# Kernel tuning notes

Measured on AMD Instinct MI355X. Metric: run time of the kernel, lower is better.

## Reference

```python
import jax, jax.numpy as jnp
import numpy as np

N, E, Nd, D, F = 100000, 400000, 4096, 512, 8000
EMB = 300
NUM_LAYERS = 5


def setup_inputs() -> dict:
    key = jax.random.key(0)
    ks = iter(jax.random.split(key, 24))
    x = jax.random.randint(next(ks), (N, 2), 0, 3)
    edge_index = jax.random.randint(next(ks), (2, E), 0, N)
    edge_attr = jax.random.randint(next(ks), (E, 2), 0, 3)
    dangling_idx = jax.random.randint(next(ks), (Nd,), 0, N)
    frag_batch = jnp.sort(jax.random.randint(next(ks), (N,), 0, F))
    dangling_edge_index = jax.random.randint(next(ks), (2, D), 0, Nd)
    drop_edge_attr = jax.random.randint(next(ks), (D, 2), 0, 3)
    p = lambda shape: jax.random.normal(next(ks), shape, jnp.float32) * 0.02
    return dict(
        x=x, edge_index=edge_index, edge_attr=edge_attr,
        dangling_idx=dangling_idx, frag_batch=frag_batch,
        dangling_edge_index=dangling_edge_index, drop_edge_attr=drop_edge_attr,
        atom_emb1=p((120, EMB)), atom_emb2=p((3, EMB)),
        gin_ee1=p((NUM_LAYERS, 6, EMB)), gin_ee2=p((NUM_LAYERS, 3, EMB)),
        W1=p((NUM_LAYERS, EMB, 2 * EMB)), b1=jnp.zeros((NUM_LAYERS, 2 * EMB), jnp.float32),
        W2=p((NUM_LAYERS, 2 * EMB, EMB)), b2=jnp.zeros((NUM_LAYERS, EMB), jnp.float32),
        bn_g=jnp.ones((NUM_LAYERS, EMB), jnp.float32), bn_b=jnp.zeros((NUM_LAYERS, EMB), jnp.float32),
        E1=p((6, 4 * EMB * EMB)), E2=p((3, 4 * EMB * EMB)),
    )


def _gnn(x, edge_index, edge_attr, atom_emb1, atom_emb2,
         gin_ee1, gin_ee2, W1, b1, W2, b2, bn_g, bn_b):
    # node features from two categorical embeddings
    h = atom_emb1[x[:, 0]] + atom_emb2[x[:, 1]]  # [N, EMB]
    src, dst = edge_index[0], edge_index[1]
    for l in range(NUM_LAYERS):
        ee = gin_ee1[l][edge_attr[:, 0]] + gin_ee2[l][edge_attr[:, 1]]  # [E, EMB]
        aggr = jax.ops.segment_sum(h[src] + ee, dst, num_segments=N)
        # self-loops with edge_attr = (4, 0)
        aggr = aggr + h + gin_ee1[l][4] + gin_ee2[l][0]
        h = jax.nn.relu(aggr @ W1[l] + b1[l]) @ W2[l] + b2[l]  # GIN MLP
        # BatchNorm1d (training-mode batch statistics), eps=1e-5
        mean = h.mean(axis=0)
        var = h.var(axis=0)
        h = (h - mean) * jax.lax.rsqrt(var + 1e-5) * bn_g[l] + bn_b[l]
        if l < NUM_LAYERS - 1:
            h = jax.nn.relu(h)
    return h


def reference(x, edge_index, edge_attr, dangling_idx, frag_batch,
              dangling_edge_index, drop_edge_attr,
              atom_emb1, atom_emb2, gin_ee1, gin_ee2,
              W1, b1, W2, b2, bn_g, bn_b, E1, E2):
    h = _gnn(x, edge_index, edge_attr, atom_emb1, atom_emb2,
             gin_ee1, gin_ee2, W1, b1, W2, b2, bn_g, bn_b)  # [N, EMB]
    dangling_out = h[dangling_idx]  # [Nd, EMB]
    # global_mean_pool over fragments
    seg_sum = jax.ops.segment_sum(h, frag_batch, num_segments=F)
    cnt = jax.ops.segment_sum(jnp.ones((N, 1), h.dtype), frag_batch, num_segments=F)
    frag_mean = seg_sum / jnp.maximum(cnt, 1.0)
    frag_out = frag_mean[frag_batch][dangling_idx]  # [Nd, EMB]
    out = jnp.concatenate([dangling_out, frag_out], axis=1) / EMB  # [Nd, 2*EMB]
    out0 = out[dangling_edge_index[0]]  # [D, 2*EMB]
    # per-edge dynamic weight matrices [D, 2*EMB, 2*EMB]
    pm = (E1[drop_edge_attr[:, 0]] + E2[drop_edge_attr[:, 1]]).reshape(D, 2 * EMB, 2 * EMB)
    out0 = jnp.einsum('dk,dkm->dm', out0, pm)
    out1 = out[dangling_edge_index[1]]
    out2 = jnp.roll(out1, 1, axis=0)  # shift_k fixed to 1 for determinism
    logits = jnp.concatenate([jnp.sum(out0 * out1, axis=1),
                              jnp.sum(out0 * out2, axis=1)], axis=0)  # [2*D]
    return logits
```

## Files before the change

kernel.cpp:

```cpp
#include <hip/hip_runtime.h>
#include <hip/hip_bf16.h>
#include <stdint.h>

#define NN 100000
#define EE 400000
#define ND 4096
#define DD 512
#define FF 8000
#define EMB 300
#define HID 600
#define NL 5
#define TCH 50176
#define MPAD 100096

typedef unsigned short u16;
typedef _Float16 f16x8 __attribute__((ext_vector_type(8)));
typedef float f32x4 __attribute__((ext_vector_type(4)));

static __device__ inline u16 f2h(float v) {
    union { _Float16 h; u16 u; } c; c.h = (_Float16)v; return c.u;
}
static __device__ inline float h2f(u16 u) {
    union { u16 u; _Float16 h; } c; c.u = u; return (float)c.h;
}
static __device__ inline uint32_t pk2(float a, float b) {
    return (uint32_t)f2h(a) | ((uint32_t)f2h(b) << 16);
}
static __device__ inline int loff(int row, int cb) {
    return row * 32 + ((cb ^ ((row >> 1) & 3)) * 8);
}

static __global__ void k_init_h(const int* __restrict__ x, const float* __restrict__ ae1,
                                const float* __restrict__ ae2, uint32_t* __restrict__ h) {
    int idx = blockIdx.x * 256 + threadIdx.x;
    if (idx >= NN * 160) return;
    int n = idx / 160, cw = idx - n * 160;
    int c = 2 * cw;
    int x0 = x[2 * n], x1 = x[2 * n + 1];
    float v0 = 0.f, v1 = 0.f;
    if (c < EMB)     v0 = ae1[x0 * EMB + c] + ae2[x1 * EMB + c];
    if (c + 1 < EMB) v1 = ae1[x0 * EMB + c + 1] + ae2[x1 * EMB + c + 1];
    h[idx] = pk2(v0, v1);
}

static __global__ void k_count(const int* __restrict__ ei, const int* __restrict__ ea,
                               int* __restrict__ deg, int* __restrict__ cnt1, int* __restrict__ cnt2) {
    int e = blockIdx.x * 256 + threadIdx.x;
    if (e >= EE) return;
    int dst = ei[EE + e];
    atomicAdd(&deg[dst], 1);
    atomicAdd(&cnt1[dst * 3 + ea[2 * e]], 1);
    atomicAdd(&cnt2[dst * 3 + ea[2 * e + 1]], 1);
}

static __global__ void k_scan1(const int* __restrict__ in, int* __restrict__ incl,
                               int* __restrict__ bsum, int L) {
    __shared__ int s[256];
    int t = threadIdx.x, i = blockIdx.x * 256 + t;
    int v = (i < L) ? in[i] : 0;
    s[t] = v; __syncthreads();
    for (int o = 1; o < 256; o <<= 1) {
        int xv = (t >= o) ? s[t - o] : 0; __syncthreads();
        s[t] += xv; __syncthreads();
    }
    if (i < L) incl[i] = s[t];
    if (t == 255) bsum[blockIdx.x] = s[255];
}

static __global__ void k_scan2(const int* __restrict__ bsum, int* __restrict__ boff, int nb) {
    __shared__ int s[1024];
    int t = threadIdx.x;
    int v = (t < nb) ? bsum[t] : 0;
    s[t] = v; __syncthreads();
    for (int o = 1; o < 1024; o <<= 1) {
        int xv = (t >= o) ? s[t - o] : 0; __syncthreads();
        s[t] += xv; __syncthreads();
    }
    if (t < nb) boff[t] = s[t] - v;
}

static __global__ void k_scan3(const int* __restrict__ in, const int* __restrict__ incl,
                               const int* __restrict__ boff, int* __restrict__ op,
                               int* __restrict__ cursor, int L) {
    int i = blockIdx.x * 256 + threadIdx.x;
    if (i >= L) return;
    int ex = incl[i] - in[i] + boff[i / 256];
    op[i] = ex;
    if (cursor) cursor[i] = ex;
    if (i == L - 1) op[L] = ex + in[i];
}

static __global__ void k_scatter(const int* __restrict__ ei, int* __restrict__ cursor,
                                 int* __restrict__ col) {
    int e = blockIdx.x * 256 + threadIdx.x;
    if (e >= EE) return;
    int dst = ei[EE + e], src = ei[e];
    int p = atomicAdd(&cursor[dst], 1);
    col[p] = src;
}

static __global__ void k_aggr(const u16* __restrict__ h, u16* __restrict__ ag,
                              const int* __restrict__ rowptr, const int* __restrict__ col,
                              const int* __restrict__ cnt1, const int* __restrict__ cnt2,
                              const float* __restrict__ ge1l, const float* __restrict__ ge2l,
                              const float* __restrict__ scv, int relu) {
    __shared__ float se[7 * 320];
    for (int idx = threadIdx.x; idx < 7 * 320; idx += 256) {
        int g = idx / 320, c = idx - g * 320;
        float v = 0.f;
        if (c < EMB) {
            if (g < 3) v = ge1l[g * EMB + c];
            else if (g < 6) v = ge2l[(g - 3) * EMB + c];
            else v = ge1l[4 * EMB + c] + ge2l[c];
        }
        se[idx] = v;
    }
    __syncthreads();
    int wv = threadIdx.x >> 6, lane = threadIdx.x & 63;
    int n = blockIdx.x * 4 + wv;
    if (n >= NN) return;
    float c1a = (float)cnt1[n * 3], c1b = (float)cnt1[n * 3 + 1], c1c = (float)cnt1[n * 3 + 2];
    float c2a = (float)cnt2[n * 3], c2b = (float)cnt2[n * 3 + 1], c2c = (float)cnt2[n * 3 + 2];

    int cw[3];
    float sc0[3], sh0[3], sc1[3], sh1[3];
    float acc0[3], acc1[3];
    const uint32_t* hn = (const uint32_t*)(h + (size_t)n * 320);
#pragma unroll
    for (int j = 0; j < 3; j++) {
        cw[j] = lane + 64 * j;
        if (cw[j] < 160) {
            int c = 2 * cw[j];
            if (scv) { sc0[j] = scv[c]; sh0[j] = scv[320 + c]; sc1[j] = scv[c + 1]; sh1[j] = scv[321 + c]; }
            else     { sc0[j] = 1.f; sh0[j] = 0.f; sc1[j] = 1.f; sh1[j] = 0.f; }
            uint32_t hv = hn[cw[j]];
            float v0 = h2f((u16)(hv & 0xffff)) * sc0[j] + sh0[j];
            float v1 = h2f((u16)(hv >> 16))    * sc1[j] + sh1[j];
            if (relu) { v0 = fmaxf(v0, 0.f); v1 = fmaxf(v1, 0.f); }
            acc0[j] = v0 + se[6 * 320 + c]
                    + c1a * se[c] + c1b * se[320 + c] + c1c * se[640 + c]
                    + c2a * se[960 + c] + c2b * se[1280 + c] + c2c * se[1600 + c];
            acc1[j] = v1 + se[6 * 320 + c + 1]
                    + c1a * se[c + 1] + c1b * se[321 + c] + c1c * se[641 + c]
                    + c2a * se[961 + c] + c2b * se[1281 + c] + c2c * se[1601 + c];
        }
    }
    int beg = rowptr[n], end = rowptr[n + 1];
    for (int p = beg; p < end; ++p) {
        const uint32_t* hr = (const uint32_t*)(h + (size_t)col[p] * 320);
#pragma unroll
        for (int j = 0; j < 3; j++) {
            if (cw[j] < 160) {
                uint32_t hv = hr[cw[j]];
                float v0 = h2f((u16)(hv & 0xffff)) * sc0[j] + sh0[j];
                float v1 = h2f((u16)(hv >> 16))    * sc1[j] + sh1[j];
                if (relu) { v0 = fmaxf(v0, 0.f); v1 = fmaxf(v1, 0.f); }
                acc0[j] += v0; acc1[j] += v1;
            }
        }
    }
    uint32_t* ao = (uint32_t*)(ag + (size_t)n * 320);
#pragma unroll
    for (int j = 0; j < 3; j++)
        if (cw[j] < 160) ao[cw[j]] = pk2(acc0[j], acc1[j]);
}

static __global__ void k_packW1(const float* __restrict__ W1, u16* __restrict__ W1p) {
    int idx = blockIdx.x * 256 + threadIdx.x;
    const int per = 640 * 320;
    if (idx >= NL * per) return;
    int l = idx / per, rem = idx % per;
    int n = rem / 320, k = rem % 320;
    float v = (k < EMB && n < HID) ? W1[(size_t)l * EMB * HID + (size_t)k * HID + n] : 0.f;
    W1p[idx] = f2h(v);
}

static __global__ void k_packW2(const float* __restrict__ W2, u16* __restrict__ W2p) {
    int idx = blockIdx.x * 256 + threadIdx.x;
    const int per = 384 * 640;
    if (idx >= NL * per) return;
    int l = idx / per, rem = idx % per;
    int n = rem / 640, k = rem % 640;
    float v = (k < HID && n < EMB) ? W2[(size_t)l * HID * EMB + (size_t)k * EMB + n] : 0.f;
    W2p[idx] = f2h(v);
}

static __global__ void k_packb(const float* __restrict__ b1, const float* __restrict__ b2,
                               float* __restrict__ b1p, float* __restrict__ b2p) {
    int idx = blockIdx.x * 256 + threadIdx.x;
    if (idx < NL * 640) {
        int l = idx / 640, n = idx % 640;
        b1p[idx] = (n < HID) ? b1[l * HID + n] : 0.f;
    } else if (idx < NL * 640 + NL * 384) {
        int j = idx - NL * 640;
        int l = j / 384, n = j % 384;
        b2p[j] = (n < EMB) ? b2[l * EMB + n] : 0.f;
    }
}

static __global__ void k_precompMt(const float* __restrict__ E1, const float* __restrict__ E2,
                                   u16* __restrict__ Mpt) {
    __shared__ float sT[32][33];
    int p = blockIdx.x, mt = blockIdx.y, kt = blockIdx.z;
    int a = p / 3, b = p % 3;
    const float* e1 = E1 + (size_t)a * 360000;
    const float* e2 = E2 + (size_t)b * 360000;
    int tx = threadIdx.x & 31, ty = threadIdx.x >> 5;
#pragma unroll
    for (int it = 0; it < 4; it++) {
        int k = kt * 32 + ty + it * 8;
        int m = mt * 32 + tx;
        float v = 0.f;
        if (k < HID && m < HID) v = e1[k * HID + m] + e2[k * HID + m];
        sT[ty + it * 8][tx] = v;
    }
    __syncthreads();
#pragma unroll
    for (int it = 0; it < 4; it++) {
        int m = mt * 32 + ty + it * 8;
        int k = kt * 32 + tx;
        Mpt[(size_t)p * 640 * 640 + (size_t)m * 640 + k] = f2h(sT[tx][ty + it * 8]);
    }
}

template <int MODE>
static __global__ __launch_bounds__(256) void k_mfma(
        const u16* __restrict__ A, const u16* __restrict__ B,
        const float* __restrict__ bias, u16* __restrict__ Out, int Mc,
        float* __restrict__ colsum, float* __restrict__ colsq) {
    constexpr int BM    = (MODE == 1) ? 128 : 64;
    constexpr int STR   = (MODE == 1) ? 320 : 640;
    constexpr int STRO  = (MODE == 1) ? 640 : 320;
    constexpr int NSTEP = (MODE == 1) ? 10 : 20;
    constexpr int MF = 4;
    constexpr int NF = (MODE == 1) ? 4 : 2;

    __shared__ __align__(16) u16 sA[BM * 32];
    __shared__ __align__(16) u16 sB[128 * 32];

    int tid = threadIdx.x;
    int lane = tid & 63, wv = tid >> 6;
    int wm = (MODE == 1) ? (wv >> 1) : 0;
    int wn = (MODE == 1) ? (wv & 1) : wv;
    int m0 = blockIdx.y * BM;
    int n0 = blockIdx.x * 128;
    int sr = tid >> 2, scb = tid & 3;

    uint4 rA0, rA1, rB0, rB1;
    auto do_load = [&](int ks) {
        int kk = ks * 32;
        const u16* as = A + (size_t)(m0 + sr) * STR + kk + scb * 8;
        rA0 = *(const uint4*)as;
        if (MODE == 1) rA1 = *(const uint4*)(as + (size_t)64 * STR);
        const u16* bs = B + (size_t)(n0 + sr) * STR + kk + scb * 8;
        rB0 = *(const uint4*)bs;
        rB1 = *(const uint4*)(bs + (size_t)64 * STR);
    };
    do_load(0);

    f32x4 acc[MF][NF];
#pragma unroll
    for (int i = 0; i < MF; i++)
#pragma unroll
        for (int j = 0; j < NF; j++) {
            acc[i][j][0] = 0.f; acc[i][j][1] = 0.f; acc[i][j][2] = 0.f; acc[i][j][3] = 0.f;
        }

    int lrow = lane & 15, lcb = lane >> 4;
    for (int ks = 0; ks < NSTEP; ++ks) {
        __syncthreads();
        *(uint4*)&sA[loff(sr, scb)] = rA0;
        if (MODE == 1) *(uint4*)&sA[loff(sr + 64, scb)] = rA1;
        *(uint4*)&sB[loff(sr, scb)] = rB0;
        *(uint4*)&sB[loff(sr + 64, scb)] = rB1;
        __syncthreads();
        if (ks + 1 < NSTEP) do_load(ks + 1);
        f16x8 af[MF], bfr[NF];
#pragma unroll
        for (int mf = 0; mf < MF; ++mf) {
            int r = wm * 64 + mf * 16 + lrow;
            af[mf] = *(const f16x8*)&sA[loff(r, lcb)];
        }
#pragma unroll
        for (int nf = 0; nf < NF; ++nf) {
            int r = wn * (NF * 16) + nf * 16 + lrow;
            bfr[nf] = *(const f16x8*)&sB[loff(r, lcb)];
        }
#pragma unroll
        for (int mf = 0; mf < MF; ++mf)
#pragma unroll
            for (int nf = 0; nf < NF; ++nf)
                acc[mf][nf] = __builtin_amdgcn_mfma_f32_16x16x32_f16(af[mf], bfr[nf], acc[mf][nf], 0, 0, 0);
    }

    int lrow4 = (lane >> 4) * 4, lcol = lane & 15;
    if (MODE == 1) {
#pragma unroll
        for (int mf = 0; mf < MF; ++mf)
#pragma unroll
            for (int nf = 0; nf < NF; ++nf) {
                int colg = n0 + wn * 64 + nf * 16 + lcol;
                float bv = bias[colg];
#pragma unroll
                for (int rg = 0; rg < 4; ++rg) {
                    int rowl = m0 + wm * 64 + mf * 16 + lrow4 + rg;
                    float v = fmaxf(acc[mf][nf][rg] + bv, 0.f);
                    Out[(size_t)rowl * STRO + colg] = f2h(v);
                }
            }
    } else {
#pragma unroll
        for (int nf = 0; nf < NF; ++nf) {
            int colg = n0 + wn * 32 + nf * 16 + lcol;
            float bv = bias[colg];
            float s = 0.f, q = 0.f;
#pragma unroll
            for (int mf = 0; mf < MF; ++mf)
#pragma unroll
                for (int rg = 0; rg < 4; ++rg) {
                    int rowl = m0 + mf * 16 + lrow4 + rg;
                    float v = acc[mf][nf][rg] + bv;
                    if (rowl < Mc) {
                        s += v; q += v * v;
                        if (colg < EMB) Out[(size_t)rowl * STRO + colg] = f2h(v);
                    }
                }
            s += __shfl_xor(s, 16); s += __shfl_xor(s, 32);
            q += __shfl_xor(q, 16); q += __shfl_xor(q, 32);
            if (lane < 16) { atomicAdd(&colsum[colg], s); atomicAdd(&colsq[colg], q); }
        }
    }
}

static __global__ void k_bnfinal(const float* __restrict__ colsum, const float* __restrict__ colsq,
                                 const float* __restrict__ g, const float* __restrict__ b,
                                 float* __restrict__ scv) {
    int c = threadIdx.x;
    if (c >= 320) return;
    if (c >= EMB) { scv[c] = 0.f; scv[320 + c] = 0.f; return; }
    float mean = colsum[c] * (1.f / NN);
    float var = colsq[c] * (1.f / NN) - mean * mean;
    float rs = rsqrtf(var + 1e-5f);
    float sc = rs * g[c];
    scv[c] = sc;
    scv[320 + c] = b[c] - mean * sc;
}

static __global__ void k_fragcnt(const int* __restrict__ fb, int* __restrict__ fcnt) {
    int i = blockIdx.x * 256 + threadIdx.x;
    if (i >= NN) return;
    atomicAdd(&fcnt[fb[i]], 1);
}

static __global__ void k_fragmean(const u16* __restrict__ h, const int* __restrict__ fstart,
                                  const float* __restrict__ scv, float* __restrict__ fm) {
    int wv = threadIdx.x >> 6, lane = threadIdx.x & 63;
    int f = blockIdx.x * 4 + wv;
    if (f >= FF) return;
    int beg = fstart[f], end = fstart[f + 1];
    float inv = (end > beg) ? 1.f / (float)(end - beg) : 0.f;
    float a0[3], a1[3]; int cw[3];
#pragma unroll
    for (int j = 0; j < 3; j++) { cw[j] = lane + 64 * j; a0[j] = 0.f; a1[j] = 0.f; }
    for (int r = beg; r < end; ++r) {
        const uint32_t* hr = (const uint32_t*)(h + (size_t)r * 320);
#pragma unroll
        for (int j = 0; j < 3; j++)
            if (cw[j] < 160) {
                uint32_t hv = hr[cw[j]];
                a0[j] += h2f((u16)(hv & 0xffff)); a1[j] += h2f((u16)(hv >> 16));
            }
    }
#pragma unroll
    for (int j = 0; j < 3; j++) {
        int c = 2 * cw[j];
        if (c < EMB)
            fm[(size_t)f * EMB + c] = (end > beg) ? (a0[j] * inv * scv[c] + scv[320 + c]) : 0.f;
        if (c + 1 < EMB)
            fm[(size_t)f * EMB + c + 1] = (end > beg) ? (a1[j] * inv * scv[c + 1] + scv[321 + c]) : 0.f;
    }
}

static __global__ void k_build_out(const u16* __restrict__ h, const float* __restrict__ fm,
                                   const int* __restrict__ didx, const int* __restrict__ fb,
                                   const float* __restrict__ scv, u16* __restrict__ outb16) {
    int idx = blockIdx.x * 256 + threadIdx.x;
    if (idx >= ND * 640) return;
    int d = idx / 640, c = idx - d * 640;
    int n = didx[d];
    float v = 0.f;
    if (c < EMB)          v = (h2f(h[(size_t)n * 320 + c]) * scv[c] + scv[320 + c]) * (1.f / EMB);
    else if (c < 2 * EMB) v = fm[(size_t)fb[n] * EMB + (c - EMB)] * (1.f / EMB);
    outb16[idx] = f2h(v);
}

static __global__ void k_bucket(const int* __restrict__ dea, int* __restrict__ eord,
                                int* __restrict__ tm, int* __restrict__ ntl) {
    __shared__ int cnt[9], off[9], cur[9];
    __shared__ short pe[DD];
    int tid = threadIdx.x;
    for (int i = tid; i < 768; i += 256) eord[i] = -1;
    if (tid < 9) { cnt[tid] = 0; cur[tid] = 0; }
    __syncthreads();
    for (int e = tid; e < DD; e += 256) {
        int p = dea[2 * e] * 3 + dea[2 * e + 1];
        pe[e] = (short)p;
        atomicAdd(&cnt[p], 1);
    }
    __syncthreads();
    if (tid == 0) {
        int o = 0, tt = 0;
        for (int p = 0; p < 9; p++) {
            off[p] = o;
            int nt = (cnt[p] + 15) >> 4;
            for (int t = 0; t < nt; t++) { tm[2 * tt] = p; tm[2 * tt + 1] = o + 16 * t; tt++; }
            o += nt * 16;
        }
        *ntl = tt;
    }
    __syncthreads();
    for (int e = tid; e < DD; e += 256) {
        int p = pe[e];
        int slot = off[p] + atomicAdd(&cur[p], 1);
        eord[slot] = e;
    }
}

static __global__ void k_vgather(const u16* __restrict__ outb16, const int* __restrict__ eord,
                                 const int* __restrict__ dei, u16* __restrict__ Vg) {
    int idx = blockIdx.x * 256 + threadIdx.x;
    if (idx >= 768 * 80) return;
    int slot = idx / 80, cb = idx - slot * 80;
    int d = eord[slot];
    uint4 v = {0u, 0u, 0u, 0u};
    if (d >= 0) v = *(const uint4*)&outb16[(size_t)dei[d] * 640 + cb * 8];
    *(uint4*)&Vg[(size_t)slot * 640 + cb * 8] = v;
}

static __global__ __launch_bounds__(256) void k_out0m(
        const u16* __restrict__ Vg, const u16* __restrict__ Mpt,
        const int* __restrict__ tm, const int* __restrict__ ntl,
        const int* __restrict__ eord, float* __restrict__ o0) {
    int bx = blockIdx.x;
    if (bx >= *ntl) return;
    int p = tm[2 * bx], row0 = tm[2 * bx + 1];
    __shared__ __align__(16) u16 sA[16 * 32];
    __shared__ __align__(16) u16 sB[640 * 32];
    int tid = threadIdx.x, lane = tid & 63, wv = tid >> 6;
    const u16* Bb = Mpt + (size_t)p * 640 * 640;
    f32x4 acc[10];
#pragma unroll
    for (int j = 0; j < 10; j++) { acc[j][0]=0.f; acc[j][1]=0.f; acc[j][2]=0.f; acc[j][3]=0.f; }
    int lrow = lane & 15, lcb = lane >> 4;
    for (int ks = 0; ks < 20; ks++) {
        int kk = ks * 32;
        __syncthreads();
        if (tid < 64) {
            int row = tid >> 2, cb = tid & 3;
            *(uint4*)&sA[loff(row, cb)] = *(const uint4*)&Vg[(size_t)(row0 + row) * 640 + kk + cb * 8];
        }
#pragma unroll
        for (int j = 0; j < 10; j++) {
            int i = tid + j * 256, row = i >> 2, cb = i & 3;
            *(uint4*)&sB[loff(row, cb)] = *(const uint4*)&Bb[(size_t)row * 640 + kk + cb * 8];
        }
        __syncthreads();
        f16x8 af = *(const f16x8*)&sA[loff(lrow, lcb)];
#pragma unroll
        for (int nf = 0; nf < 10; nf++) {
            f16x8 bf = *(const f16x8*)&sB[loff(wv * 160 + nf * 16 + lrow, lcb)];
            acc[nf] = __builtin_amdgcn_mfma_f32_16x16x32_f16(af, bf, acc[nf], 0, 0, 0);
        }
    }
    int lrow4 = (lane >> 4) * 4, lcol = lane & 15;
#pragma unroll
    for (int nf = 0; nf < 10; nf++) {
        int col = wv * 160 + nf * 16 + lcol;
#pragma unroll
        for (int rg = 0; rg < 4; rg++) {
            int row = lrow4 + rg;
            int e = eord[row0 + row];
            if (e >= 0 && col < HID) o0[(size_t)e * 640 + col] = acc[nf][rg];
        }
    }
}

static __global__ void k_logits(const float* __restrict__ o0, const u16* __restrict__ outb16,
                                const int* __restrict__ dei, float* __restrict__ dout) {
    int d = blockIdx.x;
    int tid = threadIdx.x, lane = tid & 63;
    int which = tid >> 6;
    int dsel = which ? (d + DD - 1) % DD : d;
    const float* a = o0 + (size_t)d * 640;
    const u16* bv = outb16 + (size_t)dei[DD + dsel] * 640;
    float s = 0.f;
    for (int c = lane; c < HID; c += 64) s += a[c] * h2f(bv[c]);
    for (int o = 32; o > 0; o >>= 1) s += __shfl_down(s, o);
    if (lane == 0) dout[which ? DD + d : d] = s;
}

extern "C" void kernel_launch(void* const* d_in, const int* in_sizes, int n_in,
                              void* d_out, int out_size, void* d_ws, size_t ws_size,
                              hipStream_t stream) {
    const int* x    = (const int*)d_in[0];
    const int* ei   = (const int*)d_in[1];
    const int* ea   = (const int*)d_in[2];
    const int* didx = (const int*)d_in[3];
    const int* fb   = (const int*)d_in[4];
    const int* dei  = (const int*)d_in[5];
    const int* dea  = (const int*)d_in[6];
    const float* ae1 = (const float*)d_in[7];
    const float* ae2 = (const float*)d_in[8];
    const float* ge1 = (const float*)d_in[9];
    const float* ge2 = (const float*)d_in[10];
    const float* W1  = (const float*)d_in[11];
    const float* b1  = (const float*)d_in[12];
    const float* W2  = (const float*)d_in[13];
    const float* b2  = (const float*)d_in[14];
    const float* bng = (const float*)d_in[15];
    const float* bnb = (const float*)d_in[16];
    const float* E1  = (const float*)d_in[17];
    const float* E2  = (const float*)d_in[18];
    float* dout = (float*)d_out;

    char* w = (char*)d_ws;
    auto alloc = [&](size_t bytes) -> void* {
        void* p = (void*)w;
        w += (bytes + 255) & ~(size_t)255;
        return p;
    };
    u16* h   = (u16*)alloc((size_t)MPAD * 320 * 2);
    u16* ag  = (u16*)alloc((size_t)MPAD * 320 * 2);
    u16* t   = (u16*)alloc((size_t)TCH * 640 * 2);
    u16* W1p = (u16*)alloc((size_t)NL * 640 * 320 * 2);
    u16* W2p = (u16*)alloc((size_t)NL * 384 * 640 * 2);
    u16* Mpt = (u16*)alloc((size_t)9 * 640 * 640 * 2);
    float* b1p = (float*)alloc((size_t)NL * 640 * 4);
    float* b2p = (float*)alloc((size_t)NL * 384 * 4);
    int* rowptr = (int*)alloc((size_t)(NN + 1) * 4);
    int* cursor = (int*)alloc((size_t)NN * 4);
    int* col    = (int*)alloc((size_t)EE * 4);
    int* deg    = (int*)alloc((size_t)NN * 4);
    int* cnt1   = (int*)alloc((size_t)NN * 3 * 4);
    int* cnt2   = (int*)alloc((size_t)NN * 3 * 4);
    int* incl   = (int*)alloc((size_t)NN * 4);
    int* bsum   = (int*)alloc(4096);
    int* boff   = (int*)alloc(4096);
    int* fcnt   = (int*)alloc((size_t)FF * 4);
    int* fstart = (int*)alloc((size_t)(FF + 1) * 4);
    float* colsum = (float*)alloc(384 * 4);
    float* colsq  = (float*)alloc(384 * 4);
    float* scv    = (float*)alloc(640 * 4);
    int* eord = (int*)alloc(768 * 4);
    int* tm   = (int*)alloc(96 * 4);
    int* ntl  = (int*)alloc(256);
    char* ov = (char*)t;
    auto oalloc = [&](size_t bytes) -> void* {
        void* p = (void*)ov;
        ov += (bytes + 255) & ~(size_t)255;
        return p;
    };
    float* fragmean = (float*)oalloc((size_t)FF * EMB * 4);
    u16* outb16     = (u16*)oalloc((size_t)ND * 640 * 2);
    float* o0       = (float*)oalloc((size_t)DD * 640 * 4);
    u16* Vg         = (u16*)oalloc((size_t)768 * 640 * 2);

    hipMemsetAsync(deg, 0, (size_t)NN * 4, stream);
    hipMemsetAsync(cnt1, 0, (size_t)NN * 3 * 4, stream);
    hipMemsetAsync(cnt2, 0, (size_t)NN * 3 * 4, stream);
    hipMemsetAsync(fcnt, 0, (size_t)FF * 4, stream);

    k_packW1<<<(NL * 640 * 320 + 255) / 256, 256, 0, stream>>>(W1, W1p);
    k_packW2<<<(NL * 384 * 640 + 255) / 256, 256, 0, stream>>>(W2, W2p);
    k_packb<<<(NL * (640 + 384) + 255) / 256, 256, 0, stream>>>(b1, b2, b1p, b2p);
    k_precompMt<<<dim3(9, 20, 20), 256, 0, stream>>>(E1, E2, Mpt);
    k_bucket<<<1, 256, 0, stream>>>(dea, eord, tm, ntl);

    k_init_h<<<(NN * 160 + 255) / 256, 256, 0, stream>>>(x, ae1, ae2, (uint32_t*)h);
    k_count<<<(EE + 255) / 256, 256, 0, stream>>>(ei, ea, deg, cnt1, cnt2);

    int nb = (NN + 255) / 256;
    k_scan1<<<nb, 256, 0, stream>>>(deg, incl, bsum, NN);
    k_scan2<<<1, 1024, 0, stream>>>(bsum, boff, nb);
    k_scan3<<<nb, 256, 0, stream>>>(deg, incl, boff, rowptr, cursor, NN);
    k_scatter<<<(EE + 255) / 256, 256, 0, stream>>>(ei, cursor, col);

    k_fragcnt<<<nb, 256, 0, stream>>>(fb, fcnt);
    int nbf = (FF + 255) / 256;
    k_scan1<<<nbf, 256, 0, stream>>>(fcnt, incl, bsum, FF);
    k_scan2<<<1, 1024, 0, stream>>>(bsum, boff, nbf);
    k_scan3<<<nbf, 256, 0, stream>>>(fcnt, incl, boff, fstart, (int*)nullptr, FF);

    for (int l = 0; l < NL; l++) {
        const float* ge1l = ge1 + (size_t)l * 6 * EMB;
        const float* ge2l = ge2 + (size_t)l * 3 * EMB;
        k_aggr<<<(NN + 3) / 4, 256, 0, stream>>>(h, ag, rowptr, col, cnt1, cnt2, ge1l, ge2l,
                                                 (l == 0) ? nullptr : scv, (l == 0) ? 0 : 1);
        hipMemsetAsync(colsum, 0, 384 * 4, stream);
        hipMemsetAsync(colsq, 0, 384 * 4, stream);
        for (int c0 = 0; c0 < NN; c0 += TCH) {
            int Mc = (NN - c0 < TCH) ? (NN - c0) : TCH;
            int mt1 = (Mc + 127) / 128;
            k_mfma<1><<<dim3(5, mt1), 256, 0, stream>>>(
                ag + (size_t)c0 * 320, W1p + (size_t)l * 640 * 320, b1p + l * 640,
                t, Mc, nullptr, nullptr);
            int mt2 = (Mc + 63) / 64;
            k_mfma<2><<<dim3(3, mt2), 256, 0, stream>>>(
                t, W2p + (size_t)l * 384 * 640, b2p + l * 384,
                h + (size_t)c0 * 320, Mc, colsum, colsq);
        }
        k_bnfinal<<<1, 320, 0, stream>>>(colsum, colsq, bng + (size_t)l * EMB, bnb + (size_t)l * EMB, scv);
    }

    k_fragmean<<<(FF + 3) / 4, 256, 0, stream>>>(h, fstart, scv, fragmean);
    k_build_out<<<(ND * 640 + 255) / 256, 256, 0, stream>>>(h, fragmean, didx, fb, scv, outb16);
    k_vgather<<<(768 * 80 + 255) / 256, 256, 0, stream>>>(outb16, eord, dei, Vg);
    k_out0m<<<48, 256, 0, stream>>>(Vg, Mpt, tm, ntl, eord, o0);
    k_logits<<<DD, 128, 0, stream>>>(o0, outb16, dei, dout);
}
```

Baseline: 2.058 ms.

## Use direct global-to-LDS double-buffered loads and full-width tile in MFMA GEMMs

```diff
diff --git a/kernel.cpp b/kernel.cpp
--- a/kernel.cpp
+++ b/kernel.cpp
@@ -28,6 +28,11 @@
 }
 static __device__ inline int loff(int row, int cb) {
     return row * 32 + ((cb ^ ((row >> 1) & 3)) * 8);
+}
+static __device__ inline void gll16(const u16* g, u16* l) {
+    __builtin_amdgcn_global_load_lds(
+        (const __attribute__((address_space(1))) uint32_t*)g,
+        (__attribute__((address_space(3))) uint32_t*)l, 16, 0, 0);
 }
 
 static __global__ void k_init_h(const int* __restrict__ x, const float* __restrict__ ae1,
@@ -228,35 +233,52 @@
         const u16* __restrict__ A, const u16* __restrict__ B,
         const float* __restrict__ bias, u16* __restrict__ Out, int Mc,
         float* __restrict__ colsum, float* __restrict__ colsq) {
-    constexpr int BM    = (MODE == 1) ? 128 : 64;
-    constexpr int STR   = (MODE == 1) ? 320 : 640;
-    constexpr int STRO  = (MODE == 1) ? 640 : 320;
-    constexpr int NSTEP = (MODE == 1) ? 10 : 20;
+    constexpr int BM   = (MODE == 1) ? 128 : 64;
+    constexpr int BN   = (MODE == 1) ? 128 : 320;
+    constexpr int K    = (MODE == 1) ? 320 : 640;
+    constexpr int STRO = (MODE == 1) ? 640 : 320;
+    constexpr int NSTEP = K / 32;
     constexpr int MF = 4;
-    constexpr int NF = (MODE == 1) ? 4 : 2;
-
-    __shared__ __align__(16) u16 sA[BM * 32];
-    __shared__ __align__(16) u16 sB[128 * 32];
-
-    int tid = threadIdx.x;
-    int lane = tid & 63, wv = tid >> 6;
+    constexpr int NF = (MODE == 1) ? 4 : 5;
+    constexpr int ACALLS = BM * 4 / 256;
+    constexpr int BCALLS = BN * 4 / 256;
+
+    __shared__ __align__(16) u16 sA[2][BM * 32];
+    __shared__ __align__(16) u16 sB[2][BN * 32];
+
+    int tid = threadIdx.x, lane = tid & 63, wv = tid >> 6;
     int wm = (MODE == 1) ? (wv >> 1) : 0;
     int wn = (MODE == 1) ? (wv & 1) : wv;
     int m0 = blockIdx.y * BM;
-    int n0 = blockIdx.x * 128;
-    int sr = tid >> 2, scb = tid & 3;
-
-    uint4 rA0, rA1, rB0, rB1;
-    auto do_load = [&](int ks) {
+    int n0 = (MODE == 1) ? blockIdx.x * 128 : 0;
+
+    const u16* Abase = A + (size_t)m0 * K;
+    const u16* Bbase = B + (size_t)n0 * K;
+
+    auto stageA = [&](int buf, int ks) {
         int kk = ks * 32;
-        const u16* as = A + (size_t)(m0 + sr) * STR + kk + scb * 8;
-        rA0 = *(const uint4*)as;
-        if (MODE == 1) rA1 = *(const uint4*)(as + (size_t)64 * STR);
-        const u16* bs = B + (size_t)(n0 + sr) * STR + kk + scb * 8;
-        rB0 = *(const uint4*)bs;
-        rB1 = *(const uint4*)(bs + (size_t)64 * STR);
+#pragma unroll
+        for (int j = 0; j < ACALLS; j++) {
+            int idx = j * 256 + tid;
+            int row = idx >> 2, cb = idx & 3;
+            int cb2 = cb ^ ((row >> 1) & 3);
+            gll16(Abase + (size_t)row * K + kk + cb2 * 8,
+                  &sA[buf][(size_t)(j * 256 + wv * 64) * 8]);
+        }
     };
-    do_load(0);
+    auto stageB = [&](int buf, int ks) {
+        int kk = ks * 32;
+#pragma unroll
+        for (int j = 0; j < BCALLS; j++) {
+            int idx = j * 256 + tid;
+            int row = idx >> 2, cb = idx & 3;
+            int cb2 = cb ^ ((row >> 1) & 3);
+            gll16(Bbase + (size_t)row * K + kk + cb2 * 8,
+                  &sB[buf][(size_t)(j * 256 + wv * 64) * 8]);
+        }
+    };
+
+    stageA(0, 0); stageB(0, 0);
 
     f32x4 acc[MF][NF];
 #pragma unroll
@@ -267,30 +289,27 @@
         }
 
     int lrow = lane & 15, lcb = lane >> 4;
+    int cur = 0;
     for (int ks = 0; ks < NSTEP; ++ks) {
         __syncthreads();
-        *(uint4*)&sA[loff(sr, scb)] = rA0;
-        if (MODE == 1) *(uint4*)&sA[loff(sr + 64, scb)] = rA1;
-        *(uint4*)&sB[loff(sr, scb)] = rB0;
-        *(uint4*)&sB[loff(sr + 64, scb)] = rB1;
-        __syncthreads();
-        if (ks + 1 < NSTEP) do_load(ks + 1);
+        if (ks + 1 < NSTEP) { stageA(cur ^ 1, ks + 1); stageB(cur ^ 1, ks + 1); }
         f16x8 af[MF], bfr[NF];
 #pragma unroll
         for (int mf = 0; mf < MF; ++mf) {
             int r = wm * 64 + mf * 16 + lrow;
-            af[mf] = *(const f16x8*)&sA[loff(r, lcb)];
+            af[mf] = *(const f16x8*)&sA[cur][loff(r, lcb)];
         }
 #pragma unroll
         for (int nf = 0; nf < NF; ++nf) {
             int r = wn * (NF * 16) + nf * 16 + lrow;
-            bfr[nf] = *(const f16x8*)&sB[loff(r, lcb)];
+            bfr[nf] = *(const f16x8*)&sB[cur][loff(r, lcb)];
         }
 #pragma unroll
         for (int mf = 0; mf < MF; ++mf)
 #pragma unroll
             for (int nf = 0; nf < NF; ++nf)
                 acc[mf][nf] = __builtin_amdgcn_mfma_f32_16x16x32_f16(af[mf], bfr[nf], acc[mf][nf], 0, 0, 0);
+        cur ^= 1;
     }
 
     int lrow4 = (lane >> 4) * 4, lcol = lane & 15;
@@ -311,7 +330,7 @@
     } else {
 #pragma unroll
         for (int nf = 0; nf < NF; ++nf) {
-            int colg = n0 + wn * 32 + nf * 16 + lcol;
+            int colg = wn * 80 + nf * 16 + lcol;
             float bv = bias[colg];
             float s = 0.f, q = 0.f;
 #pragma unroll
@@ -605,7 +624,7 @@
                 ag + (size_t)c0 * 320, W1p + (size_t)l * 640 * 320, b1p + l * 640,
                 t, Mc, nullptr, nullptr);
             int mt2 = (Mc + 63) / 64;
-            k_mfma<2><<<dim3(3, mt2), 256, 0, stream>>>(
+            k_mfma<2><<<dim3(1, mt2), 256, 0, stream>>>(
                 t, W2p + (size_t)l * 384 * 640, b2p + l * 384,
                 h + (size_t)c0 * 320, Mc, colsum, colsq);
         }
```

Result: slower. 2.195 ms (+6.7%).

## Apply BatchNorm+ReLU once per node and remap GEMM grid to M-major order

Applied to the files above, without the earlier changes.

```diff
diff --git a/kernel.cpp b/kernel.cpp
--- a/kernel.cpp
+++ b/kernel.cpp
@@ -102,8 +102,7 @@
 static __global__ void k_aggr(const u16* __restrict__ h, u16* __restrict__ ag,
                               const int* __restrict__ rowptr, const int* __restrict__ col,
                               const int* __restrict__ cnt1, const int* __restrict__ cnt2,
-                              const float* __restrict__ ge1l, const float* __restrict__ ge2l,
-                              const float* __restrict__ scv, int relu) {
+                              const float* __restrict__ ge1l, const float* __restrict__ ge2l) {
     __shared__ float se[7 * 320];
     for (int idx = threadIdx.x; idx < 7 * 320; idx += 256) {
         int g = idx / 320, c = idx - g * 320;
@@ -123,7 +122,6 @@
     float c2a = (float)cnt2[n * 3], c2b = (float)cnt2[n * 3 + 1], c2c = (float)cnt2[n * 3 + 2];
 
     int cw[3];
-    float sc0[3], sh0[3], sc1[3], sh1[3];
     float acc0[3], acc1[3];
     const uint32_t* hn = (const uint32_t*)(h + (size_t)n * 320);
 #pragma unroll
@@ -131,16 +129,11 @@
         cw[j] = lane + 64 * j;
         if (cw[j] < 160) {
             int c = 2 * cw[j];
-            if (scv) { sc0[j] = scv[c]; sh0[j] = scv[320 + c]; sc1[j] = scv[c + 1]; sh1[j] = scv[321 + c]; }
-            else     { sc0[j] = 1.f; sh0[j] = 0.f; sc1[j] = 1.f; sh1[j] = 0.f; }
             uint32_t hv = hn[cw[j]];
-            float v0 = h2f((u16)(hv & 0xffff)) * sc0[j] + sh0[j];
-            float v1 = h2f((u16)(hv >> 16))    * sc1[j] + sh1[j];
-            if (relu) { v0 = fmaxf(v0, 0.f); v1 = fmaxf(v1, 0.f); }
-            acc0[j] = v0 + se[6 * 320 + c]
+            acc0[j] = h2f((u16)(hv & 0xffff)) + se[6 * 320 + c]
                     + c1a * se[c] + c1b * se[320 + c] + c1c * se[640 + c]
                     + c2a * se[960 + c] + c2b * se[1280 + c] + c2c * se[1600 + c];
-            acc1[j] = v1 + se[6 * 320 + c + 1]
+            acc1[j] = h2f((u16)(hv >> 16)) + se[6 * 320 + c + 1]
                     + c1a * se[c + 1] + c1b * se[321 + c] + c1c * se[641 + c]
                     + c2a * se[961 + c] + c2b * se[1281 + c] + c2c * se[1601 + c];
         }
@@ -152,10 +145,8 @@
         for (int j = 0; j < 3; j++) {
             if (cw[j] < 160) {
                 uint32_t hv = hr[cw[j]];
-                float v0 = h2f((u16)(hv & 0xffff)) * sc0[j] + sh0[j];
-                float v1 = h2f((u16)(hv >> 16))    * sc1[j] + sh1[j];
-                if (relu) { v0 = fmaxf(v0, 0.f); v1 = fmaxf(v1, 0.f); }
-                acc0[j] += v0; acc1[j] += v1;
+                acc0[j] += h2f((u16)(hv & 0xffff));
+                acc1[j] += h2f((u16)(hv >> 16));
             }
         }
     }
@@ -163,6 +154,16 @@
 #pragma unroll
     for (int j = 0; j < 3; j++)
         if (cw[j] < 160) ao[cw[j]] = pk2(acc0[j], acc1[j]);
+}
+
+static __global__ void k_bnapply(uint32_t* __restrict__ h, const float* __restrict__ scv) {
+    int idx = blockIdx.x * 256 + threadIdx.x;
+    if (idx >= NN * 160) return;
+    int cw = idx % 160, c = 2 * cw;
+    uint32_t hv = h[idx];
+    float v0 = fmaxf(h2f((u16)(hv & 0xffff)) * scv[c] + scv[320 + c], 0.f);
+    float v1 = fmaxf(h2f((u16)(hv >> 16)) * scv[c + 1] + scv[321 + c], 0.f);
+    h[idx] = pk2(v0, v1);
 }
 
 static __global__ void k_packW1(const float* __restrict__ W1, u16* __restrict__ W1p) {
@@ -227,7 +228,7 @@
 static __global__ __launch_bounds__(256) void k_mfma(
         const u16* __restrict__ A, const u16* __restrict__ B,
         const float* __restrict__ bias, u16* __restrict__ Out, int Mc,
-        float* __restrict__ colsum, float* __restrict__ colsq) {
+        float* __restrict__ colsum, float* __restrict__ colsq, int mt) {
     constexpr int BM    = (MODE == 1) ? 128 : 64;
     constexpr int STR   = (MODE == 1) ? 320 : 640;
     constexpr int STRO  = (MODE == 1) ? 640 : 320;
@@ -242,8 +243,9 @@
     int lane = tid & 63, wv = tid >> 6;
     int wm = (MODE == 1) ? (wv >> 1) : 0;
     int wn = (MODE == 1) ? (wv & 1) : wv;
-    int m0 = blockIdx.y * BM;
-    int n0 = blockIdx.x * 128;
+    int by = blockIdx.x % mt, bx = blockIdx.x / mt;
+    int m0 = by * BM;
+    int n0 = bx * 128;
     int sr = tid >> 2, scb = tid & 3;
 
     uint4 rA0, rA1, rB0, rB1;
@@ -594,22 +596,23 @@
     for (int l = 0; l < NL; l++) {
         const float* ge1l = ge1 + (size_t)l * 6 * EMB;
         const float* ge2l = ge2 + (size_t)l * 3 * EMB;
-        k_aggr<<<(NN + 3) / 4, 256, 0, stream>>>(h, ag, rowptr, col, cnt1, cnt2, ge1l, ge2l,
-                                                 (l == 0) ? nullptr : scv, (l == 0) ? 0 : 1);
+        k_aggr<<<(NN + 3) / 4, 256, 0, stream>>>(h, ag, rowptr, col, cnt1, cnt2, ge1l, ge2l);
         hipMemsetAsync(colsum, 0, 384 * 4, stream);
         hipMemsetAsync(colsq, 0, 384 * 4, stream);
         for (int c0 = 0; c0 < NN; c0 += TCH) {
             int Mc = (NN - c0 < TCH) ? (NN - c0) : TCH;
             int mt1 = (Mc + 127) / 128;
-            k_mfma<1><<<dim3(5, mt1), 256, 0, stream>>>(
+            k_mfma<1><<<5 * mt1, 256, 0, stream>>>(
                 ag + (size_t)c0 * 320, W1p + (size_t)l * 640 * 320, b1p + l * 640,
-                t, Mc, nullptr, nullptr);
+                t, Mc, nullptr, nullptr, mt1);
             int mt2 = (Mc + 63) / 64;
-            k_mfma<2><<<dim3(3, mt2), 256, 0, stream>>>(
+            k_mfma<2><<<3 * mt2, 256, 0, stream>>>(
                 t, W2p + (size_t)l * 384 * 640, b2p + l * 384,
-                h + (size_t)c0 * 320, Mc, colsum, colsq);
+                h + (size_t)c0 * 320, Mc, colsum, colsq, mt2);
         }
         k_bnfinal<<<1, 320, 0, stream>>>(colsum, colsq, bng + (size_t)l * EMB, bnb + (size_t)l * EMB, scv);
+        if (l < NL - 1)
+            k_bnapply<<<(NN * 160 + 255) / 256, 256, 0, stream>>>((uint32_t*)h, scv);
     }
 
     k_fragmean<<<(FF + 3) / 4, 256, 0, stream>>>(h, fstart, scv, fragmean);
```

After: 2.226 ms. +8.2%, slower.
